# Kernel optimization log

Hardware: AMD Instinct MI355X
Metric: run time of the kernel (lower is better)

The kernel has to match this reference:

```python
import jax, jax.numpy as jnp
import numpy as np
from jax import lax

# --- configuration (matches init_kwargs) ---
NY_I = NX_I = 256      # interior model size
PML = 20               # pml width on each edge
DX = 4.0               # grid spacing (m)
DT = 5e-4              # time step (s); CFL: vmax*DT/DX ~ 0.4 < 0.5
NT = 64                # number of time steps
C1, C2 = 9.0 / 8.0, -1.0 / 24.0   # 4th-order staggered FD coefficients


def _shift(p, axis, off, n):
    idx = [slice(None)] * 3
    idx[axis] = slice(2 + off, 2 + off + n)
    return p[tuple(idx)]


def _dfwd(f, axis):
    # forward (half-cell +) staggered derivative, 4th order, zero halo
    pad = [(0, 0)] * 3
    pad[axis] = (2, 2)
    p = jnp.pad(f, pad)
    n = f.shape[axis]
    return (C1 * (_shift(p, axis, 1, n) - _shift(p, axis, 0, n))
            + C2 * (_shift(p, axis, 2, n) - _shift(p, axis, -1, n))) / DX


def _dbwd(f, axis):
    # backward (half-cell -) staggered derivative, 4th order, zero halo
    pad = [(0, 0)] * 3
    pad[axis] = (2, 2)
    p = jnp.pad(f, pad)
    n = f.shape[axis]
    return (C1 * (_shift(p, axis, 0, n) - _shift(p, axis, -1, n))
            + C2 * (_shift(p, axis, 1, n) - _shift(p, axis, -2, n))) / DX


def _propagate(lamb, mu, buoyancy, amps, src_loc, rec_loc):
    # replicate model edges into the PML region (as deepwave does)
    lambp = jnp.pad(lamb, PML, mode='edge')[None]      # [1,NY,NX]
    mup = jnp.pad(mu, PML, mode='edge')[None]
    buoyp = jnp.pad(buoyancy, PML, mode='edge')[None]
    NY, NX = lambp.shape[1], lambp.shape[2]
    n_shots = amps.shape[0]
    l2m = lambp + 2.0 * mup

    # CPML damping profiles (quadratic), alpha=0, kappa=1
    max_vel = lax.stop_gradient(jnp.max(jnp.sqrt(l2m * buoyp)))
    sig_max = 3.0 * max_vel * jnp.log(1000.0) / (2.0 * PML * DX)

    def prof(n):
        i = jnp.arange(n, dtype=lamb.dtype)
        d = jnp.maximum(jnp.clip(PML - i, 0.0, None),
                        jnp.clip(i - (n - 1 - PML), 0.0, None)) / PML
        return sig_max * d * d

    by = jnp.exp(-prof(NY) * DT)[None, :, None]
    ay = by - 1.0
    bx = jnp.exp(-prof(NX) * DT)[None, None, :]
    ax = bx - 1.0

    shot = jnp.arange(n_shots)[:, None]
    sl = src_loc + PML   # [S,nsrc,2]
    rl = rec_loc + PML   # [S,nrec,2]
    src_b = buoyp[0, sl[..., 0], sl[..., 1]]   # buoyancy at sources [S,nsrc]

    z = jnp.zeros((n_shots, NY, NX), lamb.dtype)
    carry0 = (z,) * 13  # vy,vx,syy,sxy,sxx, m_vyy,m_vyx,m_vxy,m_vxx, m_syyy,m_sxyy,m_sxyx,m_sxxx

    def step(carry, amp_t):
        (vy, vx, syy, sxy, sxx,
         mvyy, mvyx, mvxy, mvxx,
         msyyy, msxyy, msxyx, msxxx) = carry
        # --- velocity update ---
        d = _dbwd(syy, 1); msyyy = by * msyyy + ay * d; dsyy_y = d + msyyy
        d = _dbwd(sxy, 2); msxyx = bx * msxyx + ax * d; dsxy_x = d + msxyx
        vy = vy + DT * buoyp * (dsyy_y + dsxy_x)
        d = _dbwd(sxy, 1); msxyy = by * msxyy + ay * d; dsxy_y = d + msxyy
        d = _dbwd(sxx, 2); msxxx = bx * msxxx + ax * d; dsxx_x = d + msxxx
        vx = vx + DT * buoyp * (dsxy_y + dsxx_x)
        # --- inject y-oriented sources into vy ---
        vy = vy.at[shot, sl[..., 0], sl[..., 1]].add(DT * src_b * amp_t)
        # --- stress update ---
        d = _dfwd(vy, 1); mvyy = by * mvyy + ay * d; dvy_y = d + mvyy
        d = _dfwd(vx, 2); mvxx = bx * mvxx + ax * d; dvx_x = d + mvxx
        syy = syy + DT * (l2m * dvy_y + lambp * dvx_x)
        sxx = sxx + DT * (lambp * dvy_y + l2m * dvx_x)
        d = _dfwd(vy, 2); mvyx = bx * mvyx + ax * d; dvy_x = d + mvyx
        d = _dfwd(vx, 1); mvxy = by * mvxy + ay * d; dvx_y = d + mvxy
        sxy = sxy + DT * mup * (dvy_x + dvx_y)
        # --- record y-oriented receivers ---
        rec = vy[shot, rl[..., 0], rl[..., 1]]   # [S,nrec]
        return ((vy, vx, syy, sxy, sxx,
                 mvyy, mvyx, mvxy, mvxx,
                 msyyy, msxyy, msxyx, msxxx), rec)

    _, recs = lax.scan(step, carry0, jnp.moveaxis(amps, 2, 0))  # recs [nt,S,nrec]
    return jnp.transpose(recs, (1, 2, 0))  # [S,nrec,nt]


def setup_inputs() -> dict:
    key = jax.random.key(0)
    k = jax.random.split(key, 6)
    vp = 3000.0 + 100.0 * jax.random.normal(k[0], (NY_I, NX_I), jnp.float32)
    vs = 1500.0 + 50.0 * jax.random.normal(k[1], (NY_I, NX_I), jnp.float32)
    rho = 2200.0 + 50.0 * jax.random.normal(k[2], (NY_I, NX_I), jnp.float32)
    mu = rho * vs ** 2
    lamb = rho * (vp ** 2 - 2.0 * vs ** 2)
    buoyancy = 1.0 / rho
    source_amplitudes_y = jax.random.normal(k[3], (2, 8, NT), jnp.float32)
    source_locations_y = jax.random.randint(k[4], (2, 8, 2), 0, NY_I)
    receiver_locations_y = jax.random.randint(k[5], (2, 64, 2), 0, NY_I)
    return {
        'lamb': lamb, 'mu': mu, 'buoyancy': buoyancy,
        'source_amplitudes_y': source_amplitudes_y,
        'source_locations_y': source_locations_y,
        'receiver_locations_y': receiver_locations_y,
    }


def reference(lamb, mu, buoyancy, source_amplitudes_y,
              source_locations_y, receiver_locations_y):
    return _propagate(lamb, mu, buoyancy, source_amplitudes_y,
                      source_locations_y, receiver_locations_y)
```

## Files before the change

### kernel.cpp

```cpp
#include <hip/hip_runtime.h>
#include <math.h>

static constexpr int NYI  = 256;
static constexpr int PMLW = 20;
static constexpr int NY   = 296, NX = 296;
static constexpr int NCELL = NY * NX;
static constexpr int NS   = 2;
static constexpr int NSRC = 8;
static constexpr int NREC = 64;
static constexpr int NT   = 64;
static constexpr float DXF = 4.0f;
static constexpr float DTF = 5e-4f;
static constexpr float FC1 = 9.0f / 8.0f;
static constexpr float FC2 = -1.0f / 24.0f;
static constexpr float INV_DX = 1.0f / DXF;

static constexpr int TB = 8, TS = 37;
static constexpr int VS = TS + 4;
static constexpr int SS = TS + 8;
static constexpr int NBLK = TB * TB * NS;
static constexpr int NTHR = 512;
static constexpr int VAREA = VS * VS;
static constexpr int TAREA = TS * TS;
static constexpr int SFRAME = SS * SS - TAREA;
static constexpr int KV = 4, KT = 3;

static constexpr int GSLOT   = 3 * NS * NCELL;
static constexpr int SIG_OFF = 2 * GSLOT;
static constexpr int CNT_OFF = SIG_OFF + 32;
static constexpr int GEN_OFF = SIG_OFF + 64;

__device__ __forceinline__ float cohload(const float* p) {
    return __hip_atomic_load(p, __ATOMIC_RELAXED, __HIP_MEMORY_SCOPE_AGENT);
}
__device__ __forceinline__ void cohstore(float* p, float v) {
    __hip_atomic_store(p, v, __ATOMIC_RELAXED, __HIP_MEMORY_SCOPE_AGENT);
}

__global__ __launch_bounds__(NTHR, 1)
void elastic_fused(const float* __restrict__ lamb, const float* __restrict__ mu,
                   const float* __restrict__ buoy, const float* __restrict__ amps,
                   const int* __restrict__ src_loc, const int* __restrict__ rec_loc,
                   float* __restrict__ out, float* __restrict__ ws)
{
    __shared__ float sS[3][SS * SS];
    __shared__ float sV[2][VS * VS];
    __shared__ float byt[VS], ayt[VS], bxt[VS], axt[VS];
    __shared__ float sAmp[NSRC * NT];
    __shared__ int   rcnt;
    __shared__ short rl_r[NREC];
    __shared__ int   rl_pos[NREC];

    int* bcnt = (int*)(ws + CNT_OFF);
    int* bgen = (int*)(ws + GEN_OFF);
    float* gstr = ws;

    const int tid  = threadIdx.x;
    const int shot = blockIdx.x & 1;
    const int tb   = blockIdx.x >> 1;
    const int bty  = tb >> 3, btx = tb & 7;
    const int gy0  = bty * TS, gx0 = btx * TS;

    int bk = 0;
    auto arrive = [&]() {
        ++bk;
        __syncthreads();
        if (tid == 0) {
            int n = __hip_atomic_fetch_add(bcnt, 1, __ATOMIC_RELAXED,
                                           __HIP_MEMORY_SCOPE_AGENT) + 1;
            if (n == NBLK * bk)
                __hip_atomic_store(bgen, bk, __ATOMIC_RELAXED, __HIP_MEMORY_SCOPE_AGENT);
        }
    };
    auto wait = [&]() {
        if (tid == 0) {
            while (__hip_atomic_load(bgen, __ATOMIC_RELAXED, __HIP_MEMORY_SCOPE_AGENT) < bk)
                __builtin_amdgcn_s_sleep(1);
        }
        __syncthreads();
    };

    for (int i = tid; i < 3 * SS * SS; i += NTHR) ((float*)sS)[i] = 0.0f;
    for (int i = tid; i < 2 * VS * VS; i += NTHR) ((float*)sV)[i] = 0.0f;
    if (tid == 0) rcnt = 0;

    int   sidx_v[KV], vyv[KV], vxv[KV], smk[KV];
    float buo_v[KV];
    float msyyy[KV] = {0,0,0,0}, msxyx[KV] = {0,0,0,0};
    float msxyy[KV] = {0,0,0,0}, msxxx[KV] = {0,0,0,0};
    unsigned cvm = 0, intm = 0;
    #pragma unroll
    for (int k = 0; k < KV; ++k) {
        int vi = tid + NTHR * k;
        bool val = vi < VAREA;
        int vy_ = val ? vi / VS : 0;
        int vx_ = val ? vi - vy_ * VS : 0;
        int gy = gy0 - 2 + vy_, gx = gx0 - 2 + vx_;
        bool ing = val && gy >= 0 && gy < NY && gx >= 0 && gx < NX;
        if (ing) cvm |= 1u << k;
        if (ing && vy_ >= 4 && vy_ <= 37 && vx_ >= 4 && vx_ <= 37) intm |= 1u << k;
        vyv[k] = vy_; vxv[k] = vx_;
        sidx_v[k] = (vy_ + 2) * SS + (vx_ + 2);
        float b = 0.0f;
        if (ing) {
            int iy = min(max(gy - PMLW, 0), NYI - 1);
            int ix = min(max(gx - PMLW, 0), NYI - 1);
            b = buoy[iy * NYI + ix];
        }
        buo_v[k] = b;
        int sm = 0;
        #pragma unroll
        for (int s = 0; s < NSRC; ++s) {
            int sy = src_loc[(shot * NSRC + s) * 2 + 0] + PMLW;
            int sx = src_loc[(shot * NSRC + s) * 2 + 1] + PMLW;
            if (ing && sy == gy && sx == gx) sm |= 1 << s;
        }
        smk[k] = sm;
    }
    const unsigned bndm = cvm & ~intm;

    int   sidx_t[KT], vidx_t[KT], gidx_t[KT], tyt[KT], txt[KT];
    float lam_t[KT], mu_t[KT], l2m_t[KT];
    float mvyy[KT] = {0,0,0}, mvxx[KT] = {0,0,0}, mvyx[KT] = {0,0,0}, mvxy[KT] = {0,0,0};
    unsigned ctm = 0, ringm = 0;
    float vmax = 0.0f;
    #pragma unroll
    for (int k = 0; k < KT; ++k) {
        int ti = tid + NTHR * k;
        bool val = ti < TAREA;
        int ty = val ? ti / TS : 0;
        int tx = val ? ti - ty * TS : 0;
        int gy = gy0 + ty, gx = gx0 + tx;
        if (val) ctm |= 1u << k;
        if (val && (ty < 4 || ty >= TS - 4 || tx < 4 || tx >= TS - 4)) ringm |= 1u << k;
        tyt[k] = ty; txt[k] = tx;
        sidx_t[k] = (ty + 4) * SS + (tx + 4);
        vidx_t[k] = (ty + 2) * VS + (tx + 2);
        gidx_t[k] = gy * NX + gx;
        float la = 0.0f, m = 0.0f;
        if (val) {
            int iy = min(max(gy - PMLW, 0), NYI - 1);
            int ix = min(max(gx - PMLW, 0), NYI - 1);
            la = lamb[iy * NYI + ix];
            m  = mu  [iy * NYI + ix];
            float b = buoy[iy * NYI + ix];
            vmax = fmaxf(vmax, sqrtf((la + 2.0f * m) * b));
        }
        lam_t[k] = la; mu_t[k] = m; l2m_t[k] = la + 2.0f * m;
    }
    #pragma unroll
    for (int off = 32; off > 0; off >>= 1)
        vmax = fmaxf(vmax, __shfl_down(vmax, off));
    if ((tid & 63) == 0)
        atomicMax((int*)(ws + SIG_OFF), __float_as_int(vmax));

    bool fval[2], fin[2];
    int  flidx[2], fgi[2];
    #pragma unroll
    for (int k = 0; k < 2; ++k) {
        int ff = tid + NTHR * k;
        fval[k] = ff < SFRAME;
        int fy = 0, fx = 0;
        if (fval[k]) {
            if (ff < 4 * SS)      { fy = ff / SS;                 fx = ff - fy * SS; }
            else if (ff < 8 * SS) { int r = ff - 4 * SS; fy = SS - 4 + r / SS; fx = r % SS; }
            else {
                int r = ff - 8 * SS;
                if (r < (SS - 8) * 4) { fy = 4 + (r >> 2); fx = r & 3; }
                else { r -= (SS - 8) * 4; fy = 4 + (r >> 2); fx = SS - 4 + (r & 3); }
            }
        }
        int gy = gy0 - 4 + fy, gx = gx0 - 4 + fx;
        fin[k]   = fval[k] && gy >= 0 && gy < NY && gx >= 0 && gx < NX;
        flidx[k] = fy * SS + fx;
        fgi[k]   = fin[k] ? (gy * NX + gx) : 0;
    }

    __syncthreads();
    if (tid < NREC) {
        int r = tid;
        int ry = rec_loc[(shot * NREC + r) * 2 + 0] + PMLW;
        int rx = rec_loc[(shot * NREC + r) * 2 + 1] + PMLW;
        if (ry >= gy0 && ry < gy0 + TS && rx >= gx0 && rx < gx0 + TS) {
            int p = atomicAdd(&rcnt, 1);
            rl_r[p]   = (short)r;
            rl_pos[p] = (ry - gy0 + 2) * VS + (rx - gx0 + 2);
        }
    }
    for (int i = tid; i < NSRC * NT; i += NTHR)
        sAmp[i] = amps[shot * NSRC * NT + i];

    arrive(); wait();

    const float max_vel = __int_as_float(
        __hip_atomic_load((int*)(ws + SIG_OFF), __ATOMIC_RELAXED, __HIP_MEMORY_SCOPE_AGENT));
    const float sig_max = 3.0f * max_vel * logf(1000.0f) / (2.0f * PMLW * DXF);
    if (tid < VS) {
        auto prof = [&](int g) -> float {
            float fi = (float)g;
            float d1 = fmaxf((float)PMLW - fi, 0.0f);
            float d2 = fmaxf(fi - (float)(NY - 1 - PMLW), 0.0f);
            float dd = fmaxf(d1, d2) * (1.0f / (float)PMLW);
            return expf(-(sig_max * dd * dd) * DTF);
        };
        float b = prof(gy0 - 2 + tid); byt[tid] = b; ayt[tid] = b - 1.0f;
        b = prof(gx0 - 2 + tid);       bxt[tid] = b; axt[tid] = b - 1.0f;
    }
    __syncthreads();

    auto do_vel = [&](unsigned m, int t) {
        #pragma unroll
        for (int k = 0; k < KV; ++k) {
            if (!((m >> k) & 1)) continue;
            int si = sidx_v[k];
            float by_ = byt[vyv[k]], ay_ = ayt[vyv[k]];
            float bx_ = bxt[vxv[k]], ax_ = axt[vxv[k]];
            float d, mm;
            d = (FC1 * (sS[0][si] - sS[0][si - SS]) + FC2 * (sS[0][si + SS] - sS[0][si - 2 * SS])) * INV_DX;
            mm = by_ * msyyy[k] + ay_ * d;  msyyy[k] = mm;  float dsyy_y = d + mm;
            d = (FC1 * (sS[1][si] - sS[1][si - 1]) + FC2 * (sS[1][si + 1] - sS[1][si - 2])) * INV_DX;
            mm = bx_ * msxyx[k] + ax_ * d;  msxyx[k] = mm;  float dsxy_x = d + mm;
            d = (FC1 * (sS[1][si] - sS[1][si - SS]) + FC2 * (sS[1][si + SS] - sS[1][si - 2 * SS])) * INV_DX;
            mm = by_ * msxyy[k] + ay_ * d;  msxyy[k] = mm;  float dsxy_y = d + mm;
            d = (FC1 * (sS[2][si] - sS[2][si - 1]) + FC2 * (sS[2][si + 1] - sS[2][si - 2])) * INV_DX;
            mm = bx_ * msxxx[k] + ax_ * d;  msxxx[k] = mm;  float dsxx_x = d + mm;
            int vi = tid + NTHR * k;
            float nvy = sV[0][vi] + DTF * buo_v[k] * (dsyy_y + dsxy_x);
            float nvx = sV[1][vi] + DTF * buo_v[k] * (dsxy_y + dsxx_x);
            if (smk[k]) {
                #pragma unroll
                for (int s = 0; s < NSRC; ++s)
                    if ((smk[k] >> s) & 1) nvy += DTF * buo_v[k] * sAmp[s * NT + t];
            }
            sV[0][vi] = nvy;
            sV[1][vi] = nvx;
        }
    };

    for (int t = 0; t < NT; ++t) {
        const float* gsr = gstr + ((t + 1) & 1) * GSLOT;
        float*       gsw = gstr + (t & 1) * GSLOT;

        do_vel(intm, t);

        wait();

        float fr0[3], fr1[3];
        #pragma unroll
        for (int f = 0; f < 3; ++f) {
            fr0[f] = (t > 0 && fin[0]) ? cohload(&gsr[(f * NS + shot) * NCELL + fgi[0]]) : 0.0f;
            fr1[f] = (t > 0 && fin[1]) ? cohload(&gsr[(f * NS + shot) * NCELL + fgi[1]]) : 0.0f;
        }
        if (fval[0]) { sS[0][flidx[0]] = fr0[0]; sS[1][flidx[0]] = fr0[1]; sS[2][flidx[0]] = fr0[2]; }
        if (fval[1]) { sS[0][flidx[1]] = fr1[0]; sS[1][flidx[1]] = fr1[1]; sS[2][flidx[1]] = fr1[2]; }
        __syncthreads();

        do_vel(bndm, t);
        __syncthreads();

        if (tid < rcnt)
            out[(shot * NREC + rl_r[tid]) * NT + t] = sV[0][rl_pos[tid]];

        #pragma unroll
        for (int k = 0; k < KT; ++k) {
            if (!((ctm >> k) & 1)) continue;
            int si = sidx_t[k], vi = vidx_t[k];
            float by_ = byt[tyt[k] + 2], ay_ = ayt[tyt[k] + 2];
            float bx_ = bxt[txt[k] + 2], ax_ = axt[txt[k] + 2];
            float d, mm;
            d = (FC1 * (sV[0][vi + VS] - sV[0][vi]) + FC2 * (sV[0][vi + 2 * VS] - sV[0][vi - VS])) * INV_DX;
            mm = by_ * mvyy[k] + ay_ * d;  mvyy[k] = mm;  float dvy_y = d + mm;
            d = (FC1 * (sV[1][vi + 1] - sV[1][vi]) + FC2 * (sV[1][vi + 2] - sV[1][vi - 1])) * INV_DX;
            mm = bx_ * mvxx[k] + ax_ * d;  mvxx[k] = mm;  float dvx_x = d + mm;
            float nsyy = sS[0][si] + DTF * (l2m_t[k] * dvy_y + lam_t[k] * dvx_x);
            float nsxx = sS[2][si] + DTF * (lam_t[k] * dvy_y + l2m_t[k] * dvx_x);
            d = (FC1 * (sV[0][vi + 1] - sV[0][vi]) + FC2 * (sV[0][vi + 2] - sV[0][vi - 1])) * INV_DX;
            mm = bx_ * mvyx[k] + ax_ * d;  mvyx[k] = mm;  float dvy_x = d + mm;
            d = (FC1 * (sV[1][vi + VS] - sV[1][vi]) + FC2 * (sV[1][vi + 2 * VS] - sV[1][vi - VS])) * INV_DX;
            mm = by_ * mvxy[k] + ay_ * d;  mvxy[k] = mm;  float dvx_y = d + mm;
            float nsxy = sS[1][si] + DTF * mu_t[k] * (dvy_x + dvx_y);
            sS[0][si] = nsyy; sS[1][si] = nsxy; sS[2][si] = nsxx;
            if ((ringm >> k) & 1) {
                int gi = gidx_t[k];
                cohstore(&gsw[(0 * NS + shot) * NCELL + gi], nsyy);
                cohstore(&gsw[(1 * NS + shot) * NCELL + gi], nsxy);
                cohstore(&gsw[(2 * NS + shot) * NCELL + gi], nsxx);
            }
        }

        if (t < NT - 1) arrive();
    }
}

extern "C" void kernel_launch(void* const* d_in, const int* in_sizes, int n_in,
                              void* d_out, int out_size, void* d_ws, size_t ws_size,
                              hipStream_t stream) {
    const float* lamb    = (const float*)d_in[0];
    const float* mu      = (const float*)d_in[1];
    const float* buoy    = (const float*)d_in[2];
    const float* amps    = (const float*)d_in[3];
    const int*   src_loc = (const int*)d_in[4];
    const int*   rec_loc = (const int*)d_in[5];
    float* ws  = (float*)d_ws;
    float* out = (float*)d_out;

    hipMemsetAsync(ws + SIG_OFF, 0, 96 * sizeof(float), stream);

    elastic_fused<<<NBLK, NTHR, 0, stream>>>(lamb, mu, buoy, amps, src_loc, rec_loc, out, ws);
}
```

Before: 399.7 us.

## Replace grid-wide barrier with per-neighbor flags and redundant per-block vmax

Swaps the global counter/generation barrier used each time step for per-block progress flags. Each block only waits for its up-to-8 neighbor tiles of the same shot before reading halo stress. The global max-velocity reduction, which needed an initial grid barrier and an atomicMax, is now done redundantly inside every block by scanning the full model arrays. This removes all-to-all synchronization and lets blocks drift relative to each other, at the cost of every block reading the full 256x256 model three times at startup.

```diff
diff --git a/kernel.cpp b/kernel.cpp
--- a/kernel.cpp
+++ b/kernel.cpp
@@ -26,9 +26,7 @@
 static constexpr int KV = 4, KT = 3;
 
 static constexpr int GSLOT   = 3 * NS * NCELL;
-static constexpr int SIG_OFF = 2 * GSLOT;
-static constexpr int CNT_OFF = SIG_OFF + 32;
-static constexpr int GEN_OFF = SIG_OFF + 64;
+static constexpr int FLG_OFF = 2 * GSLOT;
 
 __device__ __forceinline__ float cohload(const float* p) {
     return __hip_atomic_load(p, __ATOMIC_RELAXED, __HIP_MEMORY_SCOPE_AGENT);
@@ -47,12 +45,12 @@
     __shared__ float sV[2][VS * VS];
     __shared__ float byt[VS], ayt[VS], bxt[VS], axt[VS];
     __shared__ float sAmp[NSRC * NT];
+    __shared__ float wmax[NTHR / 64];
     __shared__ int   rcnt;
     __shared__ short rl_r[NREC];
     __shared__ int   rl_pos[NREC];
 
-    int* bcnt = (int*)(ws + CNT_OFF);
-    int* bgen = (int*)(ws + GEN_OFF);
+    int* flags = (int*)(ws + FLG_OFF);
     float* gstr = ws;
 
     const int tid  = threadIdx.x;
@@ -60,29 +58,35 @@
     const int tb   = blockIdx.x >> 1;
     const int bty  = tb >> 3, btx = tb & 7;
     const int gy0  = bty * TS, gx0 = btx * TS;
-
-    int bk = 0;
-    auto arrive = [&]() {
-        ++bk;
-        __syncthreads();
-        if (tid == 0) {
-            int n = __hip_atomic_fetch_add(bcnt, 1, __ATOMIC_RELAXED,
-                                           __HIP_MEMORY_SCOPE_AGENT) + 1;
-            if (n == NBLK * bk)
-                __hip_atomic_store(bgen, bk, __ATOMIC_RELAXED, __HIP_MEMORY_SCOPE_AGENT);
-        }
-    };
-    auto wait = [&]() {
-        if (tid == 0) {
-            while (__hip_atomic_load(bgen, __ATOMIC_RELAXED, __HIP_MEMORY_SCOPE_AGENT) < bk)
-                __builtin_amdgcn_s_sleep(1);
-        }
-        __syncthreads();
-    };
+    const int myBlk = blockIdx.x;
+
+    int myNbr = -1;
+    if (tid < 8) {
+        int idx = tid < 4 ? tid : tid + 1;
+        int dy = idx / 3 - 1, dx = idx % 3 - 1;
+        int nty = bty + dy, ntx = btx + dx;
+        if (nty >= 0 && nty < TB && ntx >= 0 && ntx < TB)
+            myNbr = ((nty * TB + ntx) << 1) | shot;
+    }
 
     for (int i = tid; i < 3 * SS * SS; i += NTHR) ((float*)sS)[i] = 0.0f;
     for (int i = tid; i < 2 * VS * VS; i += NTHR) ((float*)sV)[i] = 0.0f;
     if (tid == 0) rcnt = 0;
+
+    float vmax = 0.0f;
+    for (int i = tid * 4; i < NYI * NYI; i += NTHR * 4) {
+        const float4 la4 = *(const float4*)(lamb + i);
+        const float4 mu4 = *(const float4*)(mu + i);
+        const float4 b4  = *(const float4*)(buoy + i);
+        vmax = fmaxf(vmax, (la4.x + 2.0f * mu4.x) * b4.x);
+        vmax = fmaxf(vmax, (la4.y + 2.0f * mu4.y) * b4.y);
+        vmax = fmaxf(vmax, (la4.z + 2.0f * mu4.z) * b4.z);
+        vmax = fmaxf(vmax, (la4.w + 2.0f * mu4.w) * b4.w);
+    }
+    #pragma unroll
+    for (int off = 32; off > 0; off >>= 1)
+        vmax = fmaxf(vmax, __shfl_down(vmax, off));
+    if ((tid & 63) == 0) wmax[tid >> 6] = vmax;
 
     int   sidx_v[KV], vyv[KV], vxv[KV], smk[KV];
     float buo_v[KV];
@@ -123,7 +127,6 @@
     float lam_t[KT], mu_t[KT], l2m_t[KT];
     float mvyy[KT] = {0,0,0}, mvxx[KT] = {0,0,0}, mvyx[KT] = {0,0,0}, mvxy[KT] = {0,0,0};
     unsigned ctm = 0, ringm = 0;
-    float vmax = 0.0f;
     #pragma unroll
     for (int k = 0; k < KT; ++k) {
         int ti = tid + NTHR * k;
@@ -143,16 +146,9 @@
             int ix = min(max(gx - PMLW, 0), NYI - 1);
             la = lamb[iy * NYI + ix];
             m  = mu  [iy * NYI + ix];
-            float b = buoy[iy * NYI + ix];
-            vmax = fmaxf(vmax, sqrtf((la + 2.0f * m) * b));
         }
         lam_t[k] = la; mu_t[k] = m; l2m_t[k] = la + 2.0f * m;
     }
-    #pragma unroll
-    for (int off = 32; off > 0; off >>= 1)
-        vmax = fmaxf(vmax, __shfl_down(vmax, off));
-    if ((tid & 63) == 0)
-        atomicMax((int*)(ws + SIG_OFF), __float_as_int(vmax));
 
     bool fval[2], fin[2];
     int  flidx[2], fgi[2];
@@ -177,23 +173,11 @@
     }
 
     __syncthreads();
-    if (tid < NREC) {
-        int r = tid;
-        int ry = rec_loc[(shot * NREC + r) * 2 + 0] + PMLW;
-        int rx = rec_loc[(shot * NREC + r) * 2 + 1] + PMLW;
-        if (ry >= gy0 && ry < gy0 + TS && rx >= gx0 && rx < gx0 + TS) {
-            int p = atomicAdd(&rcnt, 1);
-            rl_r[p]   = (short)r;
-            rl_pos[p] = (ry - gy0 + 2) * VS + (rx - gx0 + 2);
-        }
-    }
-    for (int i = tid; i < NSRC * NT; i += NTHR)
-        sAmp[i] = amps[shot * NSRC * NT + i];
-
-    arrive(); wait();
-
-    const float max_vel = __int_as_float(
-        __hip_atomic_load((int*)(ws + SIG_OFF), __ATOMIC_RELAXED, __HIP_MEMORY_SCOPE_AGENT));
+
+    float vall = wmax[0];
+    #pragma unroll
+    for (int w = 1; w < NTHR / 64; ++w) vall = fmaxf(vall, wmax[w]);
+    const float max_vel = sqrtf(vall);
     const float sig_max = 3.0f * max_vel * logf(1000.0f) / (2.0f * PMLW * DXF);
     if (tid < VS) {
         auto prof = [&](int g) -> float {
@@ -206,6 +190,18 @@
         float b = prof(gy0 - 2 + tid); byt[tid] = b; ayt[tid] = b - 1.0f;
         b = prof(gx0 - 2 + tid);       bxt[tid] = b; axt[tid] = b - 1.0f;
     }
+    if (tid < NREC) {
+        int r = tid;
+        int ry = rec_loc[(shot * NREC + r) * 2 + 0] + PMLW;
+        int rx = rec_loc[(shot * NREC + r) * 2 + 1] + PMLW;
+        if (ry >= gy0 && ry < gy0 + TS && rx >= gx0 && rx < gx0 + TS) {
+            int p = atomicAdd(&rcnt, 1);
+            rl_r[p]   = (short)r;
+            rl_pos[p] = (ry - gy0 + 2) * VS + (rx - gx0 + 2);
+        }
+    }
+    for (int i = tid; i < NSRC * NT; i += NTHR)
+        sAmp[i] = amps[shot * NSRC * NT + i];
     __syncthreads();
 
     auto do_vel = [&](unsigned m, int t) {
@@ -243,7 +239,12 @@
 
         do_vel(intm, t);
 
-        wait();
+        if (t > 0 && myNbr >= 0) {
+            while (__hip_atomic_load(&flags[myNbr], __ATOMIC_RELAXED,
+                                     __HIP_MEMORY_SCOPE_AGENT) < t)
+                __builtin_amdgcn_s_sleep(1);
+        }
+        __syncthreads();
 
         float fr0[3], fr1[3];
         #pragma unroll
@@ -288,7 +289,10 @@
             }
         }
 
-        if (t < NT - 1) arrive();
+        __syncthreads();
+        if (tid == 0 && t < NT - 1)
+            __hip_atomic_store(&flags[myBlk], t + 1, __ATOMIC_RELAXED,
+                               __HIP_MEMORY_SCOPE_AGENT);
     }
 }
 
@@ -304,7 +308,7 @@
     float* ws  = (float*)d_ws;
     float* out = (float*)d_out;
 
-    hipMemsetAsync(ws + SIG_OFF, 0, 96 * sizeof(float), stream);
+    hipMemsetAsync(ws + FLG_OFF, 0, NBLK * sizeof(int), stream);
 
     elastic_fused<<<NBLK, NTHR, 0, stream>>>(lamb, mu, buoy, amps, src_loc, rec_loc, out, ws);
 }
```

Measured after the change: 341.3 us, median of 2. 14.6% less time.
